# Optimization experiments

Measured on AMD Instinct MI355X. Metric: run time of the kernel, lower is better.

The kernel has to match this reference:

```python
import jax, jax.numpy as jnp
import numpy as np

B, T, C, H = 8, 2048, 1024, 64
SCALE = H ** -0.5


def setup_inputs() -> dict:
    key = jax.random.key(0)
    kx, kq, kk, kv = jax.random.split(key, 4)
    x = jax.random.normal(kx, (B, T, C), dtype=jnp.float32)
    w_q = jax.random.normal(kq, (C, H), dtype=jnp.float32) * (C ** -0.5)
    w_k = jax.random.normal(kk, (C, H), dtype=jnp.float32) * (C ** -0.5)
    w_v = jax.random.normal(kv, (C, H), dtype=jnp.float32) * (C ** -0.5)
    return {"x": x, "w_q": w_q, "w_k": w_k, "w_v": w_v}


def reference(x, w_q, w_k, w_v):
    # Projections: [B,T,C] @ [C,H] -> [B,T,H]
    q = jnp.einsum('btc,ch->bth', x, w_q)
    k = jnp.einsum('btc,ch->bth', x, w_k)
    v = jnp.einsum('btc,ch->bth', x, w_v)
    # Scaled scores [B,T,T], causal mask, softmax (dropout p=0 -> identity)
    wei = jnp.einsum('bqh,bkh->bqk', q, k) * SCALE
    tq = x.shape[1]
    causal = jnp.tril(jnp.ones((tq, tq), dtype=bool))
    wei = jnp.where(causal[None, :, :], wei, -jnp.inf)
    wei = jax.nn.softmax(wei, axis=-1)
    out = jnp.einsum('bqk,bkh->bqh', wei, v)
    return out
```

## Files before the change

kernel.cpp:

```cpp
#include <hip/hip_runtime.h>
#include <hip/hip_bf16.h>
#include <cstdint>

#define TB 8
#define TT 2048
#define TC 1024
#define TH 64

typedef __bf16 bf16;
typedef __bf16 bf16x2 __attribute__((ext_vector_type(2)));
typedef __bf16 bf16x4 __attribute__((ext_vector_type(4)));
typedef __bf16 bf16x8 __attribute__((ext_vector_type(8)));
typedef float  f32x4  __attribute__((ext_vector_type(4)));

constexpr float QSCALE = 0.125f * 1.44269504088896340736f;

__device__ __forceinline__ void gll16(const void* g, void* l) {
    __builtin_amdgcn_global_load_lds((const __attribute__((address_space(1))) unsigned int*)g,
                                     (__attribute__((address_space(3))) unsigned int*)l, 16, 0, 0);
}

#define WAIT_VM0()   __builtin_amdgcn_s_waitcnt(0x0F70)
#define WAIT_VM5()   __builtin_amdgcn_s_waitcnt(0x0F75)
#define WAIT_VM8()   __builtin_amdgcn_s_waitcnt(0x0F78)
#define WAIT_LGKM0() __builtin_amdgcn_s_waitcnt(0xC07F)

__global__ void prep_wT(const float* __restrict__ wq, const float* __restrict__ wk,
                        const float* __restrict__ wv, bf16* __restrict__ wT) {
    int idx = blockIdx.x * blockDim.x + threadIdx.x;
    if (idx >= 3 * TH * TC) return;
    int wsel = idx / (TH * TC);
    int rem  = idx % (TH * TC);
    int c = rem / TH;
    int h = rem % TH;
    const float* w = (wsel == 0) ? wq : (wsel == 1) ? wk : wv;
    wT[(size_t)wsel * TH * TC + (size_t)h * TC + c] = (bf16)w[(size_t)c * TH + h];
}

__launch_bounds__(512)
__global__ void proj(const float* __restrict__ x, const bf16* __restrict__ wT,
                     bf16* __restrict__ Q, bf16* __restrict__ K, bf16* __restrict__ VT) {
    __shared__ __align__(16) char lds[122880];
    const int tid  = threadIdx.x;
    const int wv8  = tid >> 6;
    const int lane = tid & 63;
    const int quad = lane >> 4, l16 = lane & 15;
    const int rg   = wv8 & 3;
    const int ch   = wv8 >> 2;
    const int m0   = blockIdx.x * 64;

    const float* xb = x + (size_t)m0 * TC;

    f32x4 acc[6];
#pragma unroll
    for (int g = 0; g < 6; g++) acc[g] = f32x4{0.f, 0.f, 0.f, 0.f};

    const int lr16 = lane >> 4, lc16 = lane & 15;
    const int lr8  = lane >> 3, lc8  = lane & 7;

#define STAGE(kc, bb)                                                          \
    {                                                                          \
        _Pragma("unroll")                                                      \
        for (int i = 0; i < 2; i++) {            \
            int base_row = wv8 * 8 + i * 4;                                    \
            int row = base_row + lr16;                                         \
            int c = lc16 ^ (row & 15);                                         \
            gll16(xb + (size_t)row * TC + (kc) * 64 + c * 4,                   \
                  lds + (bb) * 40960 + base_row * 256);                        \
        }                                                                      \
        _Pragma("unroll")                                                      \
        for (int j = 0; j < 3; j++) {            \
            int idx = wv8 * 3 + j;                                             \
            int w = idx >> 3;                                                  \
            int base_col = (idx & 7) * 8;                                      \
            int col = base_col + lr8;                                          \
            int c = lc8 ^ (col & 7);                                           \
            gll16(wT + (size_t)w * TH * TC + (size_t)col * TC + (kc) * 64 + c * 8, \
                  lds + (bb) * 40960 + 16384 + (w * 64 + base_col) * 128);     \
        }                                                                      \
    }

    STAGE(0, 0);
    STAGE(1, 1);
    for (int kc = 0; kc < 16; kc++) {
        const int cur = kc % 3;
        if (kc < 15) WAIT_VM5(); else WAIT_VM0();
        __builtin_amdgcn_s_barrier();
        __builtin_amdgcn_sched_barrier(0);
        if (kc + 2 < 16) STAGE(kc + 2, (kc + 2) % 3);
        const char* Xb = lds + cur * 40960;
        const char* Wb = lds + cur * 40960 + 16384;
        const int row = rg * 16 + l16;
#pragma unroll
        for (int s = 0; s < 2; s++) {
            int c1 = (s * 8 + 2 * quad) ^ l16;
            int c2 = (s * 8 + 2 * quad + 1) ^ l16;
            f32x4 a0 = *(const f32x4*)(Xb + row * 256 + c1 * 16);
            f32x4 a1 = *(const f32x4*)(Xb + row * 256 + c2 * 16);
            bf16x8 af;
            af[0] = (bf16)a0[0]; af[1] = (bf16)a0[1]; af[2] = (bf16)a0[2]; af[3] = (bf16)a0[3];
            af[4] = (bf16)a1[0]; af[5] = (bf16)a1[1]; af[6] = (bf16)a1[2]; af[7] = (bf16)a1[3];
#pragma unroll
            for (int g = 0; g < 6; g++) {
                int cg = ch * 6 + g;
                int w = cg >> 2;
                int col = (cg & 3) * 16 + l16;
                int c = (s * 4 + quad) ^ (col & 7);
                bf16x8 bq = *(const bf16x8*)(Wb + (w * 64 + col) * 128 + c * 16);
                acc[g] = __builtin_amdgcn_mfma_f32_16x16x32_bf16(af, bq, acc[g], 0, 0, 0);
            }
        }
    }

    const int mrow = m0 + rg * 16 + quad * 4;
    const int b = m0 >> 11;
    const int t = mrow & 2047;
#pragma unroll
    for (int g = 0; g < 6; g++) {
        int cg = ch * 6 + g;
        int w = cg >> 2;
        int col = (cg & 3) * 16 + l16;
        if (w == 0) {
#pragma unroll
            for (int r = 0; r < 4; r++)
                Q[(size_t)(mrow + r) * TH + col] = (bf16)(acc[g][r] * QSCALE);
        } else if (w == 1) {
#pragma unroll
            for (int r = 0; r < 4; r++)
                K[(size_t)(mrow + r) * TH + col] = (bf16)acc[g][r];
        } else {
            bf16x4 o;
#pragma unroll
            for (int r = 0; r < 4; r++) o[r] = (bf16)acc[g][r];
            *(bf16x4*)(VT + ((size_t)b * TH + col) * TT + t) = o;
        }
    }
}
#undef STAGE

__device__ __forceinline__ float packbf(float a, float b) {
    union { bf16x2 h; float f; } u;
    u.h[0] = (bf16)a; u.h[1] = (bf16)b;
    return u.f;
}

__launch_bounds__(512, 2)
__global__ void attn(const bf16* __restrict__ Q, const bf16* __restrict__ K,
                     const bf16* __restrict__ VT, float* __restrict__ out) {
    __shared__ __align__(16) char lds[131072];

    const int tid  = threadIdx.x;
    const int wv   = tid >> 6;
    const int wvl  = wv & 3;
    const int grp  = wv >> 2;
    const int lane = tid & 63;
    const int quad = lane >> 4, l16 = lane & 15;
    const int b  = blockIdx.x & 7;
    const int j  = blockIdx.x >> 3;
    const int qc = grp ? (63 - j) : j;
    const int q0 = qc * 32;

    char* Kst = lds + wv * 16384;
    char* Vst = Kst + 8192;

    const bf16* Qb = Q  + (size_t)b * TT * TH;
    const bf16* Kb = K  + (size_t)b * TT * TH;
    const bf16* Vb = VT + (size_t)b * TH * TT;

    bf16x8 bq[2][2];
#pragma unroll
    for (int qg = 0; qg < 2; qg++)
#pragma unroll
        for (int kh = 0; kh < 2; kh++)
            bq[qg][kh] = *(const bf16x8*)(Qb + (size_t)(q0 + qg * 16 + l16) * TH + kh * 32 + quad * 8);

    f32x4 accO[2][4];
#pragma unroll
    for (int qg = 0; qg < 2; qg++)
#pragma unroll
        for (int g = 0; g < 4; g++) accO[qg][g] = f32x4{0.f, 0.f, 0.f, 0.f};
    float lIp[2] = {0.f, 0.f};

    const int r8 = lane >> 3, c8 = lane & 7;
    const int r4 = lane >> 2, c4 = lane & 3;
    const int src1 = (quad & 1) * 32 + l16;
    const int src2 = src1 + 16;

#define STAGEKV(kt_, bb_)                                                       \
    {                                                                           \
        const int k0_ = (kt_) * 32;                                             \
        _Pragma("unroll")                                                       \
        for (int i = 0; i < 4; i++) {                                           \
            int t = i * 8 + r8;                                                 \
            gll16(Kb + (size_t)(k0_ + t) * 64 + ((c8 ^ r8) * 8),                \
                  Kst + (bb_) * 4096 + i * 1024);                               \
        }                                                                       \
        _Pragma("unroll")                                                       \
        for (int i = 0; i < 4; i++) {                                           \
            int h = i * 16 + r4;                                                \
            gll16(Vb + (size_t)h * TT + k0_ + ((c4 ^ quad) * 8),                \
                  Vst + (bb_) * 4096 + i * 1024);                               \
        }                                                                       \
    }

    if (wvl <= qc) {
        const int kt1 = (wvl + 4 <= qc) ? wvl + 4 : qc;
        STAGEKV(wvl, 0);
        STAGEKV(kt1, 1);
        int nit = 0;
        for (int kt = wvl; kt <= qc; kt += 4, nit++) {
            const int bb = nit & 1;
            WAIT_VM8();

            bf16x8 ka[2][2], bv[4];
#pragma unroll
            for (int g = 0; g < 2; g++) {
                int t = g * 16 + l16;
                const char* kr = Kst + bb * 4096 + t * 128;
                ka[g][0] = *(const bf16x8*)(kr + (((quad) ^ (t & 7)) << 4));
                ka[g][1] = *(const bf16x8*)(kr + (((4 + quad) ^ (t & 7)) << 4));
            }
#pragma unroll
            for (int g = 0; g < 4; g++) {
                int h = g * 16 + l16;
                bv[g] = *(const bf16x8*)(Vst + bb * 4096 + h * 64 + ((quad ^ (l16 >> 2)) << 4));
            }
            WAIT_LGKM0();
            {
                int ktn = kt + 8; if (ktn > qc) ktn = qc;
                STAGEKV(ktn, bb);
            }

            f32x4 s[2][2];
#pragma unroll
            for (int g = 0; g < 2; g++)
#pragma unroll
                for (int qg = 0; qg < 2; qg++) {
                    f32x4 t0 = f32x4{0.f, 0.f, 0.f, 0.f};
                    t0 = __builtin_amdgcn_mfma_f32_16x16x32_bf16(ka[g][0], bq[qg][0], t0, 0, 0, 0);
                    t0 = __builtin_amdgcn_mfma_f32_16x16x32_bf16(ka[g][1], bq[qg][1], t0, 0, 0, 0);
                    s[qg][g] = t0;
                }

            if (kt == qc) {
#pragma unroll
                for (int qg = 0; qg < 2; qg++) {
                    const int ql = qg * 16 + l16;
#pragma unroll
                    for (int g = 0; g < 2; g++)
#pragma unroll
                        for (int r = 0; r < 4; r++)
                            if (g * 16 + quad * 4 + r > ql) s[qg][g][r] = -3.0e38f;
                }
            }

#pragma unroll
            for (int qg = 0; qg < 2; qg++) {
                float rs = 0.f;
#pragma unroll
                for (int g = 0; g < 2; g++)
#pragma unroll
                    for (int r = 0; r < 4; r++) {
                        float p = __builtin_amdgcn_exp2f(s[qg][g][r]);
                        s[qg][g][r] = p;
                        rs += p;
                    }
                lIp[qg] += rs;
            }

#pragma unroll
            for (int qg = 0; qg < 2; qg++) {
                float p00 = packbf(s[qg][0][0], s[qg][0][1]);
                float p01 = packbf(s[qg][0][2], s[qg][0][3]);
                float p10 = packbf(s[qg][1][0], s[qg][1][1]);
                float p11 = packbf(s[qg][1][2], s[qg][1][3]);
                float A0p0 = __shfl(p00, src1), A0p1 = __shfl(p01, src1);
                float B0p0 = __shfl(p00, src2), B0p1 = __shfl(p01, src2);
                float A1p0 = __shfl(p10, src1), A1p1 = __shfl(p11, src1);
                float B1p0 = __shfl(p10, src2), B1p1 = __shfl(p11, src2);
                bool lo = quad < 2;
                union { float4 f; bf16x8 v; } u;
                u.f = make_float4(lo ? A0p0 : A1p0, lo ? A0p1 : A1p1,
                                  lo ? B0p0 : B1p0, lo ? B0p1 : B1p1);
#pragma unroll
                for (int g = 0; g < 4; g++)
                    accO[qg][g] = __builtin_amdgcn_mfma_f32_16x16x32_bf16(u.v, bv[g], accO[qg][g], 0, 0, 0);
            }
        }
    }
#undef STAGEKV

    float lI[2];
#pragma unroll
    for (int qg = 0; qg < 2; qg++) {
        float l = lIp[qg];
        l += __shfl_xor(l, 16);
        l += __shfl_xor(l, 32);
        lI[qg] = l;
    }

    WAIT_VM0();
    __syncthreads();
    float* Omg = (float*)(lds + grp * 34816);
    float* Lmg = (float*)(lds + 69632 + grp * 512);
#pragma unroll
    for (int qg = 0; qg < 2; qg++)
#pragma unroll
        for (int g = 0; g < 4; g++)
#pragma unroll
            for (int r = 0; r < 4; r++)
                Omg[(size_t)(wvl * 32 + qg * 16 + quad * 4 + r) * 68 + g * 16 + l16] = accO[qg][g][r];
    if (quad == 0) {
#pragma unroll
        for (int qg = 0; qg < 2; qg++)
            Lmg[wvl * 32 + qg * 16 + l16] = lI[qg];
    }
    __syncthreads();

#pragma unroll
    for (int p = 0; p < 2; p++) {
        const int idx = p * 512 + tid;
        const int c  = idx >> 9;
        const int wi = idx & 511;
        const int q  = wi >> 4;
        const int hs = (wi & 15) * 4;
        const float* Om = (const float*)(lds + c * 34816);
        const float* Lm = (const float*)(lds + 69632 + c * 512);
        float denom = 0.f, o0 = 0.f, o1 = 0.f, o2 = 0.f, o3 = 0.f;
#pragma unroll
        for (int w = 0; w < 4; w++) {
            denom += Lm[w * 32 + q];
            const float* op = Om + (size_t)(w * 32 + q) * 68 + hs;
            o0 += op[0]; o1 += op[1]; o2 += op[2]; o3 += op[3];
        }
        float inv = 1.f / denom;
        const int q0c = (c ? (63 - j) : j) * 32;
        *(float4*)(out + ((size_t)b * TT + q0c + q) * TH + hs) =
            make_float4(o0 * inv, o1 * inv, o2 * inv, o3 * inv);
    }
}

extern "C" void kernel_launch(void* const* d_in, const int* in_sizes, int n_in,
                              void* d_out, int out_size, void* d_ws, size_t ws_size,
                              hipStream_t stream) {
    const float* x  = (const float*)d_in[0];
    const float* wq = (const float*)d_in[1];
    const float* wk = (const float*)d_in[2];
    const float* wv = (const float*)d_in[3];

    char* ws = (char*)d_ws;
    bf16*  wT = (bf16*)(ws);
    bf16*  Q  = (bf16*)(ws + 393216);
    bf16*  K  = (bf16*)(ws + 2490368);
    bf16*  VT = (bf16*)(ws + 4587520);
    float* out = (float*)d_out;

    hipLaunchKernelGGL(prep_wT, dim3(768), dim3(256), 0, stream, wq, wk, wv, wT);
    hipLaunchKernelGGL(proj, dim3(256), dim3(512), 0, stream, x, wT, Q, K, VT);
    hipLaunchKernelGGL(attn, dim3(TB * 32), dim3(512), 0, stream, Q, K, VT, out);
}
```

Before: 125.4 us.

## Software-pipeline QK^T and softmax-PV across key tiles in attention loop

Restructures the key-tile loop so the softmax/PV stage for the previous tile runs while the LDS fragment loads for the current tile are in flight, with QK^T computed after the wait. V fragments from the previous tile are carried in registers, and a prologue plus epilogue handle the first and last tiles. The aim is to hide LDS latency and overlap MFMA and exp work across iterations. In exchange it raises register pressure from the extra live score and V fragments, and the sched_barrier limits how freely the compiler can reorder.

```diff
diff --git a/kernel.cpp b/kernel.cpp
--- a/kernel.cpp
+++ b/kernel.cpp
@@ -203,92 +203,121 @@
         }                                                                       \
     }
 
+#define LOADFRAG(KA, BV, bb_)                                                   \
+    {                                                                           \
+        _Pragma("unroll")                                                       \
+        for (int g = 0; g < 2; g++) {                                           \
+            int t = g * 16 + l16;                                               \
+            const char* kr = Kst + (bb_) * 4096 + t * 128;                      \
+            KA[g][0] = *(const bf16x8*)(kr + (((quad) ^ (t & 7)) << 4));        \
+            KA[g][1] = *(const bf16x8*)(kr + (((4 + quad) ^ (t & 7)) << 4));    \
+        }                                                                       \
+        _Pragma("unroll")                                                       \
+        for (int g = 0; g < 4; g++) {                                           \
+            int h = g * 16 + l16;                                               \
+            BV[g] = *(const bf16x8*)(Vst + (bb_) * 4096 + h * 64 + ((quad ^ (l16 >> 2)) << 4)); \
+        }                                                                       \
+    }
+
+#define QKT(KA, S)                                                              \
+    _Pragma("unroll")                                                           \
+    for (int g = 0; g < 2; g++)                                                 \
+        _Pragma("unroll")                                                       \
+        for (int qg = 0; qg < 2; qg++) {                                        \
+            f32x4 t0 = f32x4{0.f, 0.f, 0.f, 0.f};                               \
+            t0 = __builtin_amdgcn_mfma_f32_16x16x32_bf16(KA[g][0], bq[qg][0], t0, 0, 0, 0); \
+            t0 = __builtin_amdgcn_mfma_f32_16x16x32_bf16(KA[g][1], bq[qg][1], t0, 0, 0, 0); \
+            S[qg][g] = t0;                                                      \
+        }
+
+#define MASKDIAG(S)                                                             \
+    _Pragma("unroll")                                                           \
+    for (int qg = 0; qg < 2; qg++) {                                            \
+        const int ql = qg * 16 + l16;                                           \
+        _Pragma("unroll")                                                       \
+        for (int g = 0; g < 2; g++)                                             \
+            _Pragma("unroll")                                                   \
+            for (int r = 0; r < 4; r++)                                         \
+                if (g * 16 + quad * 4 + r > ql) S[qg][g][r] = -3.0e38f;         \
+    }
+
+#define SMPV(S, BV)                                                             \
+    {                                                                           \
+        _Pragma("unroll")                                                       \
+        for (int qg = 0; qg < 2; qg++) {                                        \
+            float rs = 0.f;                                                     \
+            _Pragma("unroll")                                                   \
+            for (int g = 0; g < 2; g++)                                         \
+                _Pragma("unroll")                                               \
+                for (int r = 0; r < 4; r++) {                                   \
+                    float p = __builtin_amdgcn_exp2f(S[qg][g][r]);              \
+                    S[qg][g][r] = p;                                            \
+                    rs += p;                                                    \
+                }                                                               \
+            lIp[qg] += rs;                                                      \
+        }                                                                       \
+        _Pragma("unroll")                                                       \
+        for (int qg = 0; qg < 2; qg++) {                                        \
+            float p00 = packbf(S[qg][0][0], S[qg][0][1]);                       \
+            float p01 = packbf(S[qg][0][2], S[qg][0][3]);                       \
+            float p10 = packbf(S[qg][1][0], S[qg][1][1]);                       \
+            float p11 = packbf(S[qg][1][2], S[qg][1][3]);                       \
+            float A0p0 = __shfl(p00, src1), A0p1 = __shfl(p01, src1);           \
+            float B0p0 = __shfl(p00, src2), B0p1 = __shfl(p01, src2);           \
+            float A1p0 = __shfl(p10, src1), A1p1 = __shfl(p11, src1);           \
+            float B1p0 = __shfl(p10, src2), B1p1 = __shfl(p11, src2);           \
+            bool lo = quad < 2;                                                 \
+            union { float4 f; bf16x8 v; } u;                                    \
+            u.f = make_float4(lo ? A0p0 : A1p0, lo ? A0p1 : A1p1,               \
+                              lo ? B0p0 : B1p0, lo ? B0p1 : B1p1);              \
+            _Pragma("unroll")                                                   \
+            for (int g = 0; g < 4; g++)                                         \
+                accO[qg][g] = __builtin_amdgcn_mfma_f32_16x16x32_bf16(u.v, BV[g], accO[qg][g], 0, 0, 0); \
+        }                                                                       \
+    }
+
     if (wvl <= qc) {
         const int kt1 = (wvl + 4 <= qc) ? wvl + 4 : qc;
         STAGEKV(wvl, 0);
         STAGEKV(kt1, 1);
-        int nit = 0;
-        for (int kt = wvl; kt <= qc; kt += 4, nit++) {
+
+        f32x4  sP[2][2];
+        bf16x8 bvP[4];
+
+        {
+            WAIT_VM8();
+            bf16x8 ka[2][2];
+            LOADFRAG(ka, bvP, 0);
+            WAIT_LGKM0();
+            __builtin_amdgcn_sched_barrier(0);
+            { int ktn = wvl + 8; if (ktn > qc) ktn = qc; STAGEKV(ktn, 0); }
+            QKT(ka, sP);
+            if (wvl == qc) MASKDIAG(sP);
+        }
+
+        int nit = 1;
+        for (int kt = wvl + 4; kt <= qc; kt += 4, nit++) {
             const int bb = nit & 1;
             WAIT_VM8();
-
-            bf16x8 ka[2][2], bv[4];
-#pragma unroll
-            for (int g = 0; g < 2; g++) {
-                int t = g * 16 + l16;
-                const char* kr = Kst + bb * 4096 + t * 128;
-                ka[g][0] = *(const bf16x8*)(kr + (((quad) ^ (t & 7)) << 4));
-                ka[g][1] = *(const bf16x8*)(kr + (((4 + quad) ^ (t & 7)) << 4));
-            }
-#pragma unroll
-            for (int g = 0; g < 4; g++) {
-                int h = g * 16 + l16;
-                bv[g] = *(const bf16x8*)(Vst + bb * 4096 + h * 64 + ((quad ^ (l16 >> 2)) << 4));
-            }
+            bf16x8 ka[2][2], bvC[4];
+            LOADFRAG(ka, bvC, bb);
+            SMPV(sP, bvP);
             WAIT_LGKM0();
-            {
-                int ktn = kt + 8; if (ktn > qc) ktn = qc;
-                STAGEKV(ktn, bb);
-            }
-
-            f32x4 s[2][2];
-#pragma unroll
-            for (int g = 0; g < 2; g++)
-#pragma unroll
-                for (int qg = 0; qg < 2; qg++) {
-                    f32x4 t0 = f32x4{0.f, 0.f, 0.f, 0.f};
-                    t0 = __builtin_amdgcn_mfma_f32_16x16x32_bf16(ka[g][0], bq[qg][0], t0, 0, 0, 0);
-                    t0 = __builtin_amdgcn_mfma_f32_16x16x32_bf16(ka[g][1], bq[qg][1], t0, 0, 0, 0);
-                    s[qg][g] = t0;
-                }
-
-            if (kt == qc) {
-#pragma unroll
-                for (int qg = 0; qg < 2; qg++) {
-                    const int ql = qg * 16 + l16;
-#pragma unroll
-                    for (int g = 0; g < 2; g++)
-#pragma unroll
-                        for (int r = 0; r < 4; r++)
-                            if (g * 16 + quad * 4 + r > ql) s[qg][g][r] = -3.0e38f;
-                }
-            }
-
-#pragma unroll
-            for (int qg = 0; qg < 2; qg++) {
-                float rs = 0.f;
-#pragma unroll
-                for (int g = 0; g < 2; g++)
-#pragma unroll
-                    for (int r = 0; r < 4; r++) {
-                        float p = __builtin_amdgcn_exp2f(s[qg][g][r]);
-                        s[qg][g][r] = p;
-                        rs += p;
-                    }
-                lIp[qg] += rs;
-            }
-
-#pragma unroll
-            for (int qg = 0; qg < 2; qg++) {
-                float p00 = packbf(s[qg][0][0], s[qg][0][1]);
-                float p01 = packbf(s[qg][0][2], s[qg][0][3]);
-                float p10 = packbf(s[qg][1][0], s[qg][1][1]);
-                float p11 = packbf(s[qg][1][2], s[qg][1][3]);
-                float A0p0 = __shfl(p00, src1), A0p1 = __shfl(p01, src1);
-                float B0p0 = __shfl(p00, src2), B0p1 = __shfl(p01, src2);
-                float A1p0 = __shfl(p10, src1), A1p1 = __shfl(p11, src1);
-                float B1p0 = __shfl(p10, src2), B1p1 = __shfl(p11, src2);
-                bool lo = quad < 2;
-                union { float4 f; bf16x8 v; } u;
-                u.f = make_float4(lo ? A0p0 : A1p0, lo ? A0p1 : A1p1,
-                                  lo ? B0p0 : B1p0, lo ? B0p1 : B1p1);
-#pragma unroll
-                for (int g = 0; g < 4; g++)
-                    accO[qg][g] = __builtin_amdgcn_mfma_f32_16x16x32_bf16(u.v, bv[g], accO[qg][g], 0, 0, 0);
-            }
-        }
+            __builtin_amdgcn_sched_barrier(0);
+            { int ktn = kt + 8; if (ktn > qc) ktn = qc; STAGEKV(ktn, bb); }
+            QKT(ka, sP);
+            if (kt == qc) MASKDIAG(sP);
+#pragma unroll
+            for (int g = 0; g < 4; g++) bvP[g] = bvC[g];
+        }
+
+        SMPV(sP, bvP);
     }
 #undef STAGEKV
+#undef LOADFRAG
+#undef QKT
+#undef MASKDIAG
+#undef SMPV
 
     float lI[2];
 #pragma unroll
```

New measurement: 125.1 us (median of 2 runs). No clear change (-0.2%).
